# Optimization experiments

Hardware: AMD Instinct MI355X
Metric: run time of the kernel (lower is better)

Reference implementation:

```python
import jax, jax.numpy as jnp
import numpy as np

L = 5      # n_levels
NH = 4     # num_heads
P = 4      # num_points
E = 256    # embed_dims
C = 256    # bev_dims
HB = 128
WB = 128
NQ = HB * WB
HD = E // NH
NL = 6     # num_layers
FF = 2 * E # ffn hidden


def setup_inputs() -> dict:
    key = jax.random.key(0)
    ks = jax.random.split(key, 12)
    s = 0.02
    def n(k, shape):
        return jax.random.normal(k, shape, jnp.float32) * s
    return dict(
        feat_bev=jax.random.normal(ks[0], (L, 1, C, HB, WB), jnp.float32),
        norm0_g=jnp.ones((L, C), jnp.float32), norm0_b=jnp.zeros((L, C), jnp.float32),
        in_w=n(ks[1], (C * L, E)), in_b=jnp.zeros((E,), jnp.float32),
        pos_row=n(ks[2], (HB, E // 2)), pos_col=n(ks[3], (WB, E // 2)),
        off_w=n(ks[4], (NL, E, NH * L * P * 2)), off_b=n(ks[5], (NL, NH * L * P * 2)),
        aw_w=n(ks[6], (NL, E, NH * L * P)), aw_b=jnp.zeros((NL, NH * L * P), jnp.float32),
        val_w=n(ks[7], (NL, C, E)), val_b=jnp.zeros((NL, E), jnp.float32),
        out_w=n(ks[8], (NL, E, E)), out_b=jnp.zeros((NL, E), jnp.float32),
        ln1_g=jnp.ones((NL, E), jnp.float32), ln1_b=jnp.zeros((NL, E), jnp.float32),
        ln2_g=jnp.ones((NL, E), jnp.float32), ln2_b=jnp.zeros((NL, E), jnp.float32),
        ffn_w1=n(ks[9], (NL, E, FF)), ffn_b1=jnp.zeros((NL, FF), jnp.float32),
        ffn_w2=n(ks[10], (NL, FF, E)), ffn_b2=jnp.zeros((NL, E), jnp.float32),
    )


def _ln(x, g, b):
    m = x.mean(-1, keepdims=True)
    v = ((x - m) ** 2).mean(-1, keepdims=True)
    return (x - m) * jax.lax.rsqrt(v + 1e-5) * g + b


def reference(feat_bev, norm0_g, norm0_b, in_w, in_b, pos_row, pos_col,
              off_w, off_b, aw_w, aw_b, val_w, val_b, out_w, out_b,
              ln1_g, ln1_b, ln2_g, ln2_b, ffn_w1, ffn_b1, ffn_w2, ffn_b2):
    Lv, bs, Cc, H, W = feat_bev.shape
    nq = H * W
    # per-level LN over channels (norm_layer0)
    f = feat_bev.transpose(0, 1, 3, 4, 2).reshape(Lv, bs, nq, Cc)
    f = _ln(f, norm0_g[:, None, None, :], norm0_b[:, None, None, :])  # [L, bs, nq, C]
    # input_proj on channel-concat of levels (level-major block rows of in_w)
    q = jnp.einsum('lbnc,lce->bne', f, in_w.reshape(Lv, Cc, E)) + in_b  # [bs, nq, E]
    # learned positional encoding: pos[h, w] = cat(col[w], row[h])
    pos = jnp.concatenate([
        jnp.broadcast_to(pos_col[None, :, :], (H, W, E // 2)),
        jnp.broadcast_to(pos_row[:, None, :], (H, W, E // 2))], -1).reshape(1, nq, E)
    # reference points (pixel centers, normalized)
    ys, xs = jnp.meshgrid(jnp.arange(H, dtype=jnp.float32) + 0.5,
                          jnp.arange(W, dtype=jnp.float32) + 0.5, indexing='ij')
    ref = jnp.stack([xs.ravel() / W, ys.ravel() / H], -1)  # [nq, 2] (x, y)
    norm = jnp.array([W, H], jnp.float32)
    b_ix = jnp.arange(bs)[:, None, None, None, None]
    h_ix = jnp.arange(NH)[None, None, :, None, None]
    l_ix = jnp.arange(Lv)[None, None, None, :, None]
    for i in range(NL):
        qp = q + pos
        off = (qp @ off_w[i] + off_b[i]).reshape(bs, nq, NH, Lv, P, 2)
        aw = jax.nn.softmax((qp @ aw_w[i] + aw_b[i]).reshape(bs, nq, NH, Lv * P), -1)
        aw = aw.reshape(bs, nq, NH, Lv, P)
        loc = ref[None, :, None, None, None, :] + off / norm
        x = loc[..., 0] * W - 0.5
        y = loc[..., 1] * H - 0.5
        x0 = jnp.floor(x); y0 = jnp.floor(y)
        fx = x - x0; fy = y - y0
        x0i = x0.astype(jnp.int32); y0i = y0.astype(jnp.int32)
        # per-layer value projection of normed multi-level features
        val = (jnp.einsum('lbnc,ce->blne', f, val_w[i]) + val_b[i]).reshape(bs, Lv, nq, NH, HD)
        acc = jnp.zeros((bs, nq, NH, HD), q.dtype)
        for dx, dy, wgt in ((0, 0, (1 - fx) * (1 - fy)), (1, 0, fx * (1 - fy)),
                            (0, 1, (1 - fx) * fy), (1, 1, fx * fy)):
            ix = x0i + dx; iy = y0i + dy
            valid = ((ix >= 0) & (ix < W) & (iy >= 0) & (iy < H)).astype(q.dtype)
            sidx = jnp.clip(iy, 0, H - 1) * W + jnp.clip(ix, 0, W - 1)
            g = val[b_ix, l_ix, sidx, h_ix]  # [bs, nq, NH, Lv, P, HD]
            acc = acc + jnp.einsum('bqhlp,bqhlpd->bqhd', wgt * valid * aw, g)
        q = q + (acc.reshape(bs, nq, NH * HD) @ out_w[i] + out_b[i])
        q = _ln(q, ln1_g[i], ln1_b[i])
        q = q + jax.nn.relu(q @ ffn_w1[i] + ffn_b1[i]) @ ffn_w2[i] + ffn_b2[i]
        q = _ln(q, ln2_g[i], ln2_b[i])
    return q.transpose(0, 2, 1).reshape(bs, E, H, W)
```

## Files before the change

kernel.cpp:

```cpp
#include <hip/hip_runtime.h>
#include <hip/hip_bf16.h>
#include <stdint.h>

static constexpr int kL  = 5;
static constexpr int kNH = 4;
static constexpr int kP  = 4;
static constexpr int kE  = 256;
static constexpr int kC  = 256;
static constexpr int kH  = 128;
static constexpr int kW  = 128;
static constexpr int kNQ = kH * kW;
static constexpr int kNL = 6;
static constexpr int kFF = 2 * kE;
static constexpr int kCOMB = 240;

typedef short bf16x8 __attribute__((ext_vector_type(8)));
typedef float f32x4 __attribute__((ext_vector_type(4)));

__device__ __forceinline__ short f2bf(float x) {
  union { float f; uint32_t u; } v; v.f = x;
  uint32_t r = v.u + 0x7fffu + ((v.u >> 16) & 1u);
  return (short)(r >> 16);
}
__device__ __forceinline__ uint32_t pack2(float a, float b) {
  return (uint32_t)(unsigned short)f2bf(a) | ((uint32_t)(unsigned short)f2bf(b) << 16);
}
__device__ __forceinline__ float bflo(uint32_t u) { return __uint_as_float(u << 16); }
__device__ __forceinline__ float bfhi(uint32_t u) { return __uint_as_float(u & 0xffff0000u); }
__device__ __forceinline__ float bf2f(unsigned short u) {
  return __uint_as_float((uint32_t)u << 16);
}

__device__ __forceinline__ void gl_lds16(const void* g, void* l) {
  __builtin_amdgcn_global_load_lds(
      (const __attribute__((address_space(1))) void*)g,
      (__attribute__((address_space(3))) void*)l, 16, 0, 0);
}

template <int BM, int MODE, int RB>
__global__ __launch_bounds__(512, MODE == 0 ? 4 : 2) void gemm2_kernel(
    const short* __restrict__ A, long sAb, int lda,
    const short* __restrict__ BT, int ldbt, int Kb, int nbatch,
    const float* __restrict__ bias,
    float* Cf, short* __restrict__ Cb, int ldc, int relu, long zouts,
    const float* __restrict__ pos_row, const float* __restrict__ pos_col,
    const short* __restrict__ w2BT, const float* __restrict__ w2B,
    short* __restrict__ out2) {
  static_assert(BM == 64, "layout assumes BM=64");
  constexpr bool FUSED = (MODE == 5);
  constexpr int BK = 64;
  constexpr int KG = 2;
  constexpr int NW = 8;
  constexpr int MT = 2;
  constexpr int NT = 4;
  constexpr int AG = (BM / 16) * KG;
  constexpr int BG = 16 * KG;
  constexpr int ASZ = BM * BK;
  constexpr int BSZ = 256 * BK;
  __shared__ short smem[2 * ASZ + 2 * BSZ + (FUSED ? 64 * 280 : 0)];
  short* const Asm = smem;
  short* const Bsm = smem + 2 * ASZ;
  short* const qpS = smem + 2 * ASZ + 2 * BSZ;
  const int tid = threadIdx.x;
  const int wave = tid >> 6, lane = tid & 63;
  const int wy = wave >> 2, wx = wave & 3;
  const long row0 = (long)blockIdx.y * BM;
  const int col0 = blockIdx.x * 256;
  const int srow = lane >> 2;
  const int skof = ((lane & 3) ^ (srow & 3)) * 8;
  const int fr = lane & 15, fq = lane >> 4;
  const int ua = (fr * 4 + (fq ^ (fr & 3))) * 8;
  f32x4 acc[MT][NT] = {};
  const int KT = Kb >> 6;
  const int NTILES = nbatch * KT;

  auto stage_tile = [&](int buf, int bb, int kt) {
    const short* Ab = A + (long)bb * sAb + row0 * lda;
    const short* Bb = BT + (long)col0 * ldbt + (long)bb * Kb;
    int k0 = kt * BK;
#pragma unroll
    for (int t = wave; t < AG + BG; t += NW) {
      if (t < AG) {
        int rg = t >> 1, kg = t & 1;
        gl_lds16(Ab + (long)(rg * 16 + srow) * lda + k0 + kg * 32 + skof,
                 &Asm[buf * ASZ + t * 512]);
      } else {
        int u = t - AG;
        int rg = u >> 1, kg = u & 1;
        gl_lds16(Bb + (long)(rg * 16 + srow) * ldbt + k0 + kg * 32 + skof,
                 &Bsm[buf * BSZ + u * 512]);
      }
    }
  };

  int cur = 0;
  stage_tile(0, 0, 0);
  __syncthreads();
  int sb = 0, sk = 0;
  for (int idx = 0; idx < NTILES; ++idx) {
    if (idx + 1 < NTILES) {
      if (++sk == KT) { sk = 0; ++sb; }
      stage_tile(cur ^ 1, sb, sk);
    }
#pragma unroll
    for (int kk = 0; kk < KG; ++kk) {
      bf16x8 af[MT], bfv[NT];
#pragma unroll
      for (int t = 0; t < MT; ++t)
        af[t] = *(const bf16x8*)&Asm[cur * ASZ + ((wy * MT + t) * KG + kk) * 512 + ua];
#pragma unroll
      for (int t = 0; t < NT; ++t)
        bfv[t] = *(const bf16x8*)&Bsm[cur * BSZ + ((wx * 4 + t) * KG + kk) * 512 + ua];
#pragma unroll
      for (int mt = 0; mt < MT; ++mt)
#pragma unroll
        for (int nt = 0; nt < NT; ++nt)
          acc[mt][nt] = __builtin_amdgcn_mfma_f32_16x16x32_bf16(
              af[mt], bfv[nt], acc[mt][nt], 0, 0, 0);
    }
    __syncthreads();
    cur ^= 1;
  }

  const int colb = col0 + wx * 64 + fr;
  const long rowb = row0 + wy * 32 + fq * 4;

  if (MODE == 0) {
    const long zoff = (long)blockIdx.x * zouts;
#pragma unroll
    for (int mt = 0; mt < MT; ++mt)
#pragma unroll
      for (int rr = 0; rr < 4; ++rr) {
        long row = rowb + mt * 16 + rr;
#pragma unroll
        for (int nt = 0; nt < NT; ++nt) {
          int col = colb + nt * 16;
          float v = acc[mt][nt][rr] + bias[col];
          if (relu) v = fmaxf(v, 0.f);
          if (Cf) Cf[row * ldc + col] = v;
          if (Cb) Cb[zoff + row * ldc + col] = f2bf(v);
        }
      }
  } else if (MODE == 5) {
#pragma unroll
    for (int mt = 0; mt < MT; ++mt)
#pragma unroll
      for (int rr = 0; rr < 4; ++rr) {
        long row = rowb + mt * 16 + rr;
        int rl = wy * 32 + mt * 16 + fq * 4 + rr;
        int wpos = (int)row & (kW - 1), hpos = (int)row >> 7;
#pragma unroll
        for (int nt = 0; nt < NT; ++nt) {
          int col = colb + nt * 16;
          float v = acc[mt][nt][rr] + bias[col];
          Cf[row * 256 + col] = v;
          float pv = (col < 128) ? pos_col[wpos * 128 + col]
                                 : pos_row[hpos * 128 + (col - 128)];
          qpS[rl * 280 + col] = f2bf(v + pv);
        }
      }
  }
  if constexpr (FUSED) {
    auto stageW = [&](int buf, int t2) {
      int k0 = (t2 & 3) * BK;
#pragma unroll
      for (int u = wave; u < BG; u += NW) {
        int rg = u >> 1, kg = u & 1;
        gl_lds16(w2BT + (long)(rg * 16 + srow) * 256 + k0 + kg * 32 + skof,
                 &Bsm[buf * BSZ + u * 512]);
      }
    };
    f32x4 acc2[4][NT] = {};
    stageW(cur, 0);
    __syncthreads();
    for (int t2 = 0; t2 < 4; ++t2) {
      if (t2 + 1 < 4) stageW(cur ^ 1, t2 + 1);
      int k0 = t2 * BK;
#pragma unroll
      for (int kk = 0; kk < KG; ++kk) {
        bf16x8 av[4], bv[NT];
#pragma unroll
        for (int mt = 0; mt < 4; ++mt)
          av[mt] = *(const bf16x8*)&qpS[(mt * 16 + fr) * 280 + k0 +
                                        kk * 32 + fq * 8];
#pragma unroll
        for (int t = 0; t < NT; ++t)
          bv[t] = *(const bf16x8*)&Bsm[cur * BSZ + ((wx * 4 + t) * KG + kk) *
                                           512 + ua];
#pragma unroll
        for (int mt = 0; mt < 4; ++mt)
#pragma unroll
          for (int t = 0; t < NT; ++t)
            acc2[mt][t] = __builtin_amdgcn_mfma_f32_16x16x32_bf16(
                av[mt], bv[t], acc2[mt][t], 0, 0, 0);
      }
      __syncthreads();
      cur ^= 1;
    }
#pragma unroll
    for (int mt = 0; mt < 4; ++mt)
#pragma unroll
      for (int rr = 0; rr < 4; ++rr) {
        long row = row0 + mt * 16 + fq * 4 + rr;
#pragma unroll
        for (int nt = 0; nt < NT; ++nt) {
          int oc = wx * 64 + nt * 16 + fr;
          out2[row * 256 + oc] = f2bf(acc2[mt][nt][rr] + w2B[oc]);
        }
      }
  }
}

template <int LAST>
__global__ __launch_bounds__(512, 2) void layer_kernel(
    const short* __restrict__ accb, const short* __restrict__ outTW,
    const float* __restrict__ outb, float* __restrict__ q,
    const float* __restrict__ ln1g, const float* __restrict__ ln1b,
    const short* __restrict__ f1T, const float* __restrict__ f1b,
    short* __restrict__ hid, const short* __restrict__ f2T,
    const float* __restrict__ f2b, const float* __restrict__ ln2g,
    const float* __restrict__ ln2b, const float* __restrict__ pos_row,
    const float* __restrict__ pos_col, const short* __restrict__ combTW,
    const float* __restrict__ comb_b, short* __restrict__ comb_bf) {
  constexpr int BK = 64, KG = 2, NW = 8, MT = 2, NT = 4;
  constexpr int AG = 8, BG = 32;
  constexpr int ASZ = 64 * BK, BSZ = 256 * BK;
  __shared__ short smem[2 * ASZ + 2 * BSZ + 64 * 280];
  short* const Asm = smem;
  short* const Bsm = smem + 2 * ASZ;
  short* const qpS = smem + 2 * ASZ + 2 * BSZ;
  float2* const lnpart = (float2*)Asm;
  const int tid = threadIdx.x;
  const int wave = tid >> 6, lane = tid & 63;
  const int wy = wave >> 2, wx = wave & 3;
  const long row0 = (long)blockIdx.y * 64;
  const int srow = lane >> 2;
  const int skof = ((lane & 3) ^ (srow & 3)) * 8;
  const int fr = lane & 15, fq = lane >> 4;
  const int ua = (fr * 4 + (fq ^ (fr & 3))) * 8;
  const int colb = wx * 64 + fr;
  const long rowb = row0 + wy * 32 + fq * 4;
  f32x4 acc[MT][NT];

  auto run_gemm = [&](const short* Ab, int lda, const short* Bb, int ldbt,
                      int ntiles) {
#pragma unroll
    for (int mt = 0; mt < MT; ++mt)
#pragma unroll
      for (int nt = 0; nt < NT; ++nt) acc[mt][nt] = f32x4{0.f, 0.f, 0.f, 0.f};
    auto stage = [&](int buf, int kt) {
      int k0 = kt * BK;
#pragma unroll
      for (int t = wave; t < AG + BG; t += NW) {
        if (t < AG) {
          int rg = t >> 1, kg = t & 1;
          gl_lds16(Ab + (long)(rg * 16 + srow) * lda + k0 + kg * 32 + skof,
                   &Asm[buf * ASZ + t * 512]);
        } else {
          int u = t - AG, rg = u >> 1, kg = u & 1;
          gl_lds16(Bb + (long)(rg * 16 + srow) * ldbt + k0 + kg * 32 + skof,
                   &Bsm[buf * BSZ + u * 512]);
        }
      }
    };
    stage(0, 0);
    __syncthreads();
    int cur = 0;
    for (int t = 0; t < ntiles; ++t) {
      if (t + 1 < ntiles) stage(cur ^ 1, t + 1);
#pragma unroll
      for (int kk = 0; kk < KG; ++kk) {
        bf16x8 af[MT], bfv[NT];
#pragma unroll
        for (int i = 0; i < MT; ++i)
          af[i] = *(const bf16x8*)&Asm[cur * ASZ +
                                       ((wy * MT + i) * KG + kk) * 512 + ua];
#pragma unroll
        for (int i = 0; i < NT; ++i)
          bfv[i] = *(const bf16x8*)&Bsm[cur * BSZ +
                                        ((wx * 4 + i) * KG + kk) * 512 + ua];
#pragma unroll
        for (int mt = 0; mt < MT; ++mt)
#pragma unroll
          for (int nt = 0; nt < NT; ++nt)
            acc[mt][nt] = __builtin_amdgcn_mfma_f32_16x16x32_bf16(
                af[mt], bfv[nt], acc[mt][nt], 0, 0, 0);
      }
      __syncthreads();
      cur ^= 1;
    }
  };

  auto ln_epilogue = [&](const float* bias, auto residf, const float* g,
                         const float* b, auto writer) {
#pragma unroll
    for (int mt = 0; mt < MT; ++mt)
#pragma unroll
      for (int rr = 0; rr < 4; ++rr) {
        long row = rowb + mt * 16 + rr;
        int rl = wy * 32 + mt * 16 + fq * 4 + rr;
        float s = 0.f, s2 = 0.f;
#pragma unroll
        for (int nt = 0; nt < NT; ++nt) {
          int col = colb + nt * 16;
          float v = acc[mt][nt][rr] + bias[col] + residf(row, col, rl);
          acc[mt][nt][rr] = v;
          s += v; s2 += v * v;
        }
#pragma unroll
        for (int o = 8; o > 0; o >>= 1) {
          s += __shfl_xor(s, o);
          s2 += __shfl_xor(s2, o);
        }
        if (fr == 0) lnpart[rl * 4 + wx] = make_float2(s, s2);
      }
    __syncthreads();
#pragma unroll
    for (int mt = 0; mt < MT; ++mt)
#pragma unroll
      for (int rr = 0; rr < 4; ++rr) {
        int rl = wy * 32 + mt * 16 + fq * 4 + rr;
        long row = rowb + mt * 16 + rr;
        float s = 0.f, s2 = 0.f;
#pragma unroll
        for (int c = 0; c < 4; ++c) {
          s += lnpart[rl * 4 + c].x;
          s2 += lnpart[rl * 4 + c].y;
        }
        float m = s * (1.f / 256);
        float var = s2 * (1.f / 256) - m * m;
        float rs = rsqrtf(var + 1e-5f);
#pragma unroll
        for (int nt = 0; nt < NT; ++nt) {
          int col = colb + nt * 16;
          float y = (acc[mt][nt][rr] - m) * rs * g[col] + b[col];
          writer(rl, row, col, y);
        }
      }
  };

  auto run_gemm2 = [&](const short* WT, int nhalf, int ld2, bool dorelu,
                       const float* b2, short* out2) {
    auto stageW = [&](int buf, int t2) {
      int hf = t2 >> 2, k0 = (t2 & 3) * BK;
#pragma unroll
      for (int u = wave; u < BG; u += NW) {
        int rg = u >> 1, kg = u & 1;
        gl_lds16(WT + (long)(hf * 256 + rg * 16 + srow) * 256 + k0 + kg * 32 +
                     skof,
                 &Bsm[buf * BSZ + u * 512]);
      }
    };
    const int NT2 = nhalf * 4;
    f32x4 acc2[4][NT];
#pragma unroll
    for (int mt = 0; mt < 4; ++mt)
#pragma unroll
      for (int t = 0; t < NT; ++t) acc2[mt][t] = f32x4{0.f, 0.f, 0.f, 0.f};
    stageW(0, 0);
    __syncthreads();
    int cur = 0;
    for (int t2 = 0; t2 < NT2; ++t2) {
      if (t2 + 1 < NT2) stageW(cur ^ 1, t2 + 1);
      int k0 = (t2 & 3) * BK;
#pragma unroll
      for (int kk = 0; kk < KG; ++kk) {
        bf16x8 av[4], bv[NT];
#pragma unroll
        for (int mt = 0; mt < 4; ++mt)
          av[mt] = *(const bf16x8*)&qpS[(mt * 16 + fr) * 280 + k0 + kk * 32 +
                                        fq * 8];
#pragma unroll
        for (int t = 0; t < NT; ++t)
          bv[t] = *(const bf16x8*)&Bsm[cur * BSZ +
                                       ((wx * 4 + t) * KG + kk) * 512 + ua];
#pragma unroll
        for (int mt = 0; mt < 4; ++mt)
#pragma unroll
          for (int t = 0; t < NT; ++t)
            acc2[mt][t] = __builtin_amdgcn_mfma_f32_16x16x32_bf16(
                av[mt], bv[t], acc2[mt][t], 0, 0, 0);
      }
      if ((t2 & 3) == 3) {
        int hf = t2 >> 2;
#pragma unroll
        for (int mt = 0; mt < 4; ++mt)
#pragma unroll
          for (int rr = 0; rr < 4; ++rr) {
            long row = row0 + mt * 16 + fq * 4 + rr;
#pragma unroll
            for (int nt = 0; nt < NT; ++nt) {
              int oc = hf * 256 + wx * 64 + nt * 16 + fr;
              float v = acc2[mt][nt][rr] + b2[oc];
              if (dorelu) v = fmaxf(v, 0.f);
              out2[row * ld2 + oc] = f2bf(v);
            }
          }
#pragma unroll
        for (int mt = 0; mt < 4; ++mt)
#pragma unroll
          for (int t = 0; t < NT; ++t) acc2[mt][t] = f32x4{0.f, 0.f, 0.f, 0.f};
      }
      __syncthreads();
      cur ^= 1;
    }
  };

  run_gemm(accb + row0 * 256, 256, outTW, 256, 4);
  ln_epilogue(
      outb, [&](long row, int col, int) { return q[row * 256 + col]; }, ln1g,
      ln1b,
      [&](int rl, long row, int col, float y) { qpS[rl * 280 + col] = f2bf(y); });
  run_gemm2(f1T, 2, 512, true, f1b, hid);
  run_gemm(hid + row0 * 512, 512, f2T, 512, 8);
  ln_epilogue(
      f2b,
      [&](long row, int col, int rl) {
        return bf2f((unsigned short)qpS[rl * 280 + col]);
      },
      ln2g, ln2b,
      [&](int rl, long row, int col, float y) {
        q[row * 256 + col] = y;
        if (!LAST) {
          int wpos = (int)row & (kW - 1), hpos = (int)row >> 7;
          float pv = (col < 128) ? pos_col[wpos * 128 + col]
                                 : pos_row[hpos * 128 + (col - 128)];
          qpS[rl * 280 + col] = f2bf(y + pv);
        }
      });
  if (!LAST) run_gemm2(combTW, 1, 256, false, comb_b, comb_bf);
}

__global__ __launch_bounds__(256) void convert_all_kernel(
    const float* __restrict__ in_w, const float* __restrict__ val_w,
    const float* __restrict__ out_w, const float* __restrict__ ffn_w1,
    const float* __restrict__ ffn_w2, const float* __restrict__ off_w,
    const float* __restrict__ aw_w, const float* __restrict__ off_b,
    const float* __restrict__ aw_b,
    short* __restrict__ inT, short* __restrict__ valT, short* __restrict__ outT,
    short* __restrict__ ffn1T, short* __restrict__ ffn2T,
    short* __restrict__ combT, float* __restrict__ comb_bias) {
  long e = (long)blockIdx.x * 256 + threadIdx.x;
  if (e < 327680) {
    int idx = (int)e;
    int n = idx / 1280, k = idx - n * 1280;
    inT[idx] = f2bf(in_w[(long)k * 256 + n]);
    return;
  }
  e -= 327680;
  if (e < 393216) {
    int z = (int)(e >> 16), idx = (int)e & 65535;
    int n = idx >> 8, k = idx & 255;
    valT[e] = f2bf(val_w[((long)z * 256 + k) * 256 + n]);
    return;
  }
  e -= 393216;
  if (e < 393216) {
    int z = (int)(e >> 16), idx = (int)e & 65535;
    int n = idx >> 8, k = idx & 255;
    outT[e] = f2bf(out_w[((long)z * 256 + k) * 256 + n]);
    return;
  }
  e -= 393216;
  if (e < 786432) {
    int z = (int)(e / 131072);
    int idx = (int)(e - (long)z * 131072);
    int n = idx >> 8, k = idx & 255;
    ffn1T[e] = f2bf(ffn_w1[((long)z * 256 + k) * 512 + n]);
    return;
  }
  e -= 786432;
  if (e < 786432) {
    int z = (int)(e / 131072);
    int idx = (int)(e - (long)z * 131072);
    int n = idx >> 9, k = idx & 511;
    ffn2T[e] = f2bf(ffn_w2[((long)z * 512 + k) * 256 + n]);
    return;
  }
  e -= 786432;
  {
    int z = (int)(e >> 16), idx = (int)e & 65535;
    int n = idx >> 8, k = idx & 255;
    float v = 0.f;
    if (n < 160) v = off_w[((long)z * 256 + k) * 160 + n];
    else if (n < kCOMB) v = aw_w[((long)z * 256 + k) * 80 + (n - 160)];
    combT[e] = f2bf(v);
    if (k == 0)
      comb_bias[z * 256 + n] =
          (n < 160) ? off_b[z * 160 + n]
                    : (n < kCOMB ? aw_b[z * 80 + (n - 160)] : 0.f);
  }
}

__global__ __launch_bounds__(256) void ln_fused_kernel(
    const float* __restrict__ feat, const float* __restrict__ g,
    const float* __restrict__ b, short* __restrict__ f) {
  __shared__ float tile[256][33];
  __shared__ float2 part[8][32];
  __shared__ float mS[32], rsS[32];
  int l = blockIdx.y;
  int n0 = blockIdx.x * 32;
  int tx = threadIdx.x & 31;
  int ty = threadIdx.x >> 5;
  float s = 0.f, s2 = 0.f;
#pragma unroll 8
  for (int j = 0; j < 32; ++j) {
    int c = ty * 32 + j;
    float v = feat[((long)(l * kC + c)) * kNQ + n0 + tx];
    tile[c][tx] = v;
    s += v; s2 += v * v;
  }
  part[ty][tx] = make_float2(s, s2);
  __syncthreads();
  if (ty == 0) {
    float ss = 0.f, ss2 = 0.f;
#pragma unroll
    for (int j = 0; j < 8; ++j) {
      ss += part[j][tx].x; ss2 += part[j][tx].y;
    }
    float m = ss * (1.f / kC);
    float var = ss2 * (1.f / kC) - m * m;
    mS[tx] = m;
    rsS[tx] = rsqrtf(var + 1e-5f);
  }
  __syncthreads();
  int c = threadIdx.x;
  float gv = g[l * kC + c], bv = b[l * kC + c];
#pragma unroll 8
  for (int r = 0; r < 32; ++r) {
    float v = (tile[c][r] - mS[r]) * rsS[r] * gv + bv;
    f[((long)l * kNQ + n0 + r) * kC + c] = f2bf(v);
  }
}

__global__ __launch_bounds__(256) void sample_kernel(
    const unsigned short* __restrict__ comb, const short* __restrict__ val,
    short* __restrict__ accb) {
  __shared__ float2 ic[4][2][4][85];
  int wv = threadIdx.x >> 6;
  int lane = threadIdx.x & 63;
  int half = lane >> 5;
  int hl = lane & 31;
  int n = blockIdx.x * 8 + wv * 2 + half;
  int wq = n & (kW - 1);
  int hq = n >> 7;
  const unsigned short* cb = comb + (long)n * 256;
#pragma unroll
  for (int h = 0; h < 4; ++h) {
    float raw = (hl < 20) ? bf2f(cb[160 + h * 20 + hl]) : -1e30f;
    float mx = raw;
#pragma unroll
    for (int o = 16; o > 0; o >>= 1) mx = fmaxf(mx, __shfl_xor(mx, o));
    float ev = (hl < 20) ? __expf(raw - mx) : 0.f;
    float se = ev;
#pragma unroll
    for (int o = 16; o > 0; o >>= 1) se += __shfl_xor(se, o);
    if (hl < 20) {
      float awv = ev / se;
      int l = hl >> 2;
      float ox = bf2f(cb[h * 40 + hl * 2 + 0]);
      float oy = bf2f(cb[h * 40 + hl * 2 + 1]);
      float x = (float)wq + ox;
      float y = (float)hq + oy;
      float x0f = floorf(x), y0f = floorf(y);
      float fx = x - x0f, fy = y - y0f;
      int x0 = (int)x0f, y0 = (int)y0f;
#pragma unroll
      for (int c = 0; c < 4; ++c) {
        int dx = c & 1, dy = c >> 1;
        int ix = x0 + dx, iy = y0 + dy;
        float wgt = (dx ? fx : 1.f - fx) * (dy ? fy : 1.f - fy);
        bool valid = (ix >= 0 && ix < kW && iy >= 0 && iy < kH);
        int cix = min(max(ix, 0), kW - 1);
        int ciy = min(max(iy, 0), kH - 1);
        int sidx = ciy * kW + cix;
        int byteoff = (l * kNQ + sidx) * (kE * 2);
        float coef = valid ? awv * wgt : 0.f;
        ic[wv][half][h][hl * 4 + c] = make_float2(__int_as_float(byteoff), coef);
      }
    }
  }
  __syncthreads();
  int h2 = (lane >> 3) & 3;
  int ch8 = (lane & 7) * 8;
  const char* vb = (const char*)val + (h2 * 64 + ch8) * 2;
  const float2* icp = &ic[wv][half][h2][0];
  float a0 = 0.f, a1 = 0.f, a2 = 0.f, a3 = 0.f;
  float a4 = 0.f, a5 = 0.f, a6 = 0.f, a7 = 0.f;
#pragma unroll 4
  for (int j = 0; j < 80; ++j) {
    float2 oc = icp[j];
    int off = __float_as_int(oc.x);
    uint4 u = *(const uint4*)(vb + off);
    float cf = oc.y;
    a0 += cf * bflo(u.x); a1 += cf * bfhi(u.x);
    a2 += cf * bflo(u.y); a3 += cf * bfhi(u.y);
    a4 += cf * bflo(u.z); a5 += cf * bfhi(u.z);
    a6 += cf * bflo(u.w); a7 += cf * bfhi(u.w);
  }
  uint4 o;
  o.x = pack2(a0, a1); o.y = pack2(a2, a3);
  o.z = pack2(a4, a5); o.w = pack2(a6, a7);
  *(uint4*)(accb + (long)n * kE + h2 * 64 + ch8) = o;
}

__global__ __launch_bounds__(256) void transpose_kernel(
    const float* __restrict__ q, float* __restrict__ out) {
  __shared__ float t[32][33];
  int eb = blockIdx.x * 32, nb = blockIdx.y * 32;
  int tx = threadIdx.x & 31, ty = threadIdx.x >> 5;
#pragma unroll
  for (int j = 0; j < 4; ++j)
    t[ty + j * 8][tx] = q[(long)(nb + ty + j * 8) * kE + eb + tx];
  __syncthreads();
#pragma unroll
  for (int j = 0; j < 4; ++j)
    out[(long)(eb + ty + j * 8) * kNQ + nb + tx] = t[tx][ty + j * 8];
}

extern "C" void kernel_launch(void* const* d_in, const int* in_sizes, int n_in,
                              void* d_out, int out_size, void* d_ws,
                              size_t ws_size, hipStream_t stream) {
  const float* feat    = (const float*)d_in[0];
  const float* norm0_g = (const float*)d_in[1];
  const float* norm0_b = (const float*)d_in[2];
  const float* in_w    = (const float*)d_in[3];
  const float* in_b    = (const float*)d_in[4];
  const float* pos_row = (const float*)d_in[5];
  const float* pos_col = (const float*)d_in[6];
  const float* off_w   = (const float*)d_in[7];
  const float* off_b   = (const float*)d_in[8];
  const float* aw_w    = (const float*)d_in[9];
  const float* aw_b    = (const float*)d_in[10];
  const float* val_w   = (const float*)d_in[11];
  const float* val_b   = (const float*)d_in[12];
  const float* out_w   = (const float*)d_in[13];
  const float* out_b   = (const float*)d_in[14];
  const float* ln1_g   = (const float*)d_in[15];
  const float* ln1_b   = (const float*)d_in[16];
  const float* ln2_g   = (const float*)d_in[17];
  const float* ln2_b   = (const float*)d_in[18];
  const float* ffn_w1  = (const float*)d_in[19];
  const float* ffn_b1  = (const float*)d_in[20];
  const float* ffn_w2  = (const float*)d_in[21];
  const float* ffn_b2  = (const float*)d_in[22];

  char* p = (char*)d_ws;
  auto alloc = [&](size_t bytes) -> char* {
    char* r = p;
    p += (bytes + 255) & ~(size_t)255;
    return r;
  };
  const size_t valSlab = (size_t)kL * kNQ * kE;
  short* f_bf    = (short*)alloc((size_t)kL * kNQ * kC * 2);
  short* val_bf  = (short*)alloc(3 * valSlab * 2);
  float* q       = (float*)alloc((size_t)kNQ * kE * 4);
  short* accb    = (short*)alloc((size_t)kNQ * kE * 2);
  short* hid_bf  = (short*)alloc((size_t)kNQ * kFF * 2);
  short* comb_bf = (short*)alloc((size_t)kNQ * 256 * 2);
  float* comb_b  = (float*)alloc((size_t)kNL * 256 * 4);
  short* inT     = (short*)alloc((size_t)256 * 1280 * 2);
  short* valT    = (short*)alloc((size_t)kNL * 256 * 256 * 2);
  short* outT    = (short*)alloc((size_t)kNL * 256 * 256 * 2);
  short* ffn1T   = (short*)alloc((size_t)kNL * 512 * 256 * 2);
  short* ffn2T   = (short*)alloc((size_t)kNL * 256 * 512 * 2);
  short* combT   = (short*)alloc((size_t)kNL * 256 * 256 * 2);

  convert_all_kernel<<<12032, 256, 0, stream>>>(
      in_w, val_w, out_w, ffn_w1, ffn_w2, off_w, aw_w, off_b, aw_b,
      inT, valT, outT, ffn1T, ffn2T, combT, comb_b);

  ln_fused_kernel<<<dim3(kNQ / 32, kL), 256, 0, stream>>>(feat, norm0_g,
                                                          norm0_b, f_bf);

  const long zouts = (long)kL * kNQ * 256 - 256;
  gemm2_kernel<64, 0, 0><<<dim3(3, kL * kNQ / 64), 512, 0, stream>>>(
      f_bf, 0, kC, valT, 256, 256, 1, val_b,
      nullptr, val_bf, kE, 0, zouts, nullptr, nullptr,
      nullptr, nullptr, nullptr);

  gemm2_kernel<64, 5, 0><<<dim3(1, kNQ / 64), 512, 0, stream>>>(
      f_bf, (long)kNQ * kC, kC, inT, 1280, 256, kL, in_b,
      q, nullptr, 256, 0, 0, pos_row, pos_col, combT, comb_b, comb_bf);

  for (int i = 0; i < kNL; ++i) {
    const short* outT_i  = outT + (long)i * 256 * 256;
    const short* f1T_i   = ffn1T + (long)i * 512 * 256;
    const short* f2T_i   = ffn2T + (long)i * 256 * 512;

    sample_kernel<<<kNQ / 8, 256, 0, stream>>>(
        (const unsigned short*)comb_bf, val_bf + (long)(i % 3) * valSlab,
        accb);
    if (i == 2) {
      gemm2_kernel<64, 0, 0><<<dim3(3, kL * kNQ / 64), 512, 0, stream>>>(
          f_bf, 0, kC, valT + 3 * 256 * 256, 256, 256, 1, val_b + 3 * kE,
          nullptr, val_bf, kE, 0, zouts, nullptr, nullptr,
          nullptr, nullptr, nullptr);
    }
    if (i + 1 < kNL) {
      layer_kernel<0><<<dim3(1, kNQ / 64), 512, 0, stream>>>(
          accb, outT_i, out_b + (long)i * kE, q,
          ln1_g + (long)i * kE, ln1_b + (long)i * kE,
          f1T_i, ffn_b1 + (long)i * kFF, hid_bf,
          f2T_i, ffn_b2 + (long)i * kE,
          ln2_g + (long)i * kE, ln2_b + (long)i * kE,
          pos_row, pos_col,
          combT + (long)(i + 1) * 256 * 256, comb_b + (i + 1) * 256, comb_bf);
    } else {
      layer_kernel<1><<<dim3(1, kNQ / 64), 512, 0, stream>>>(
          accb, outT_i, out_b + (long)i * kE, q,
          ln1_g + (long)i * kE, ln1_b + (long)i * kE,
          f1T_i, ffn_b1 + (long)i * kFF, hid_bf,
          f2T_i, ffn_b2 + (long)i * kE,
          ln2_g + (long)i * kE, ln2_b + (long)i * kE,
          pos_row, pos_col, nullptr, nullptr, nullptr);
    }
  }

  transpose_kernel<<<dim3(kE / 32, kNQ / 32), 256, 0, stream>>>(q,
                                                                (float*)d_out);
}
```

Before: 868.3 us.

## Fuse deformable sampling into layer kernel and feed output-projection GEMM from LDS

```diff
diff --git a/kernel.cpp b/kernel.cpp
--- a/kernel.cpp
+++ b/kernel.cpp
@@ -213,8 +213,9 @@
 
 template <int LAST>
 __global__ __launch_bounds__(512, 2) void layer_kernel(
-    const short* __restrict__ accb, const short* __restrict__ outTW,
-    const float* __restrict__ outb, float* __restrict__ q,
+    const unsigned short* __restrict__ comb, const short* __restrict__ val,
+    const short* __restrict__ outTW, const float* __restrict__ outb,
+    float* __restrict__ q,
     const float* __restrict__ ln1g, const float* __restrict__ ln1b,
     const short* __restrict__ f1T, const float* __restrict__ f1b,
     short* __restrict__ hid, const short* __restrict__ f2T,
@@ -229,6 +230,8 @@
   short* const Asm = smem;
   short* const Bsm = smem + 2 * ASZ;
   short* const qpS = smem + 2 * ASZ + 2 * BSZ;
+  short* const accS = qpS;
+  float2* const ic = (float2*)Bsm;
   float2* const lnpart = (float2*)Asm;
   const int tid = threadIdx.x;
   const int wave = tid >> 6, lane = tid & 63;
@@ -242,6 +245,127 @@
   const long rowb = row0 + wy * 32 + fq * 4;
   f32x4 acc[MT][NT];
 
+  {
+    const int half = lane >> 5;
+    const int hl = lane & 31;
+    const int h2 = (lane >> 3) & 3;
+    const int ch8 = (lane & 7) * 8;
+    const int ch = h2 * 64 + ch8;
+    const char* vb = (const char*)val + ch * 2;
+    for (int pass = 0; pass < 4; ++pass) {
+      int nl = wave * 8 + pass * 2 + half;
+      long n = row0 + nl;
+      int wq = (int)n & (kW - 1), hq = (int)n >> 7;
+      const unsigned short* cb = comb + n * 256;
+      float2* icw = ic + (long)(wave * 2 + half) * 4 * 85;
+#pragma unroll
+      for (int h = 0; h < 4; ++h) {
+        float raw = (hl < 20) ? bf2f(cb[160 + h * 20 + hl]) : -1e30f;
+        float mx = raw;
+#pragma unroll
+        for (int o = 16; o > 0; o >>= 1) mx = fmaxf(mx, __shfl_xor(mx, o));
+        float ev = (hl < 20) ? __expf(raw - mx) : 0.f;
+        float se = ev;
+#pragma unroll
+        for (int o = 16; o > 0; o >>= 1) se += __shfl_xor(se, o);
+        if (hl < 20) {
+          float awv = ev / se;
+          int l = hl >> 2;
+          float ox = bf2f(cb[h * 40 + hl * 2 + 0]);
+          float oy = bf2f(cb[h * 40 + hl * 2 + 1]);
+          float x = (float)wq + ox;
+          float y = (float)hq + oy;
+          float x0f = floorf(x), y0f = floorf(y);
+          float fx = x - x0f, fy = y - y0f;
+          int x0 = (int)x0f, y0 = (int)y0f;
+#pragma unroll
+          for (int c = 0; c < 4; ++c) {
+            int dx = c & 1, dy = c >> 1;
+            int ix = x0 + dx, iy = y0 + dy;
+            float wgt = (dx ? fx : 1.f - fx) * (dy ? fy : 1.f - fy);
+            bool valid = (ix >= 0 && ix < kW && iy >= 0 && iy < kH);
+            int cix = min(max(ix, 0), kW - 1);
+            int ciy = min(max(iy, 0), kH - 1);
+            int sidx = ciy * kW + cix;
+            int byteoff = (l * kNQ + sidx) * (kE * 2);
+            float coef = valid ? awv * wgt : 0.f;
+            icw[h * 85 + hl * 4 + c] =
+                make_float2(__int_as_float(byteoff), coef);
+          }
+        }
+      }
+      __syncthreads();
+      const float2* icp = ic + ((long)(wave * 2 + half) * 4 + h2) * 85;
+      float a0 = 0.f, a1 = 0.f, a2 = 0.f, a3 = 0.f;
+      float a4 = 0.f, a5 = 0.f, a6 = 0.f, a7 = 0.f;
+#pragma unroll 4
+      for (int j = 0; j < 80; ++j) {
+        float2 oc = icp[j];
+        int off = __float_as_int(oc.x);
+        uint4 u = *(const uint4*)(vb + off);
+        float cf = oc.y;
+        a0 += cf * bflo(u.x); a1 += cf * bfhi(u.x);
+        a2 += cf * bflo(u.y); a3 += cf * bfhi(u.y);
+        a4 += cf * bflo(u.z); a5 += cf * bfhi(u.z);
+        a6 += cf * bflo(u.w); a7 += cf * bfhi(u.w);
+      }
+      uint4 o;
+      o.x = pack2(a0, a1); o.y = pack2(a2, a3);
+      o.z = pack2(a4, a5); o.w = pack2(a6, a7);
+      int rg = nl >> 4, sr = nl & 15, kg = ch >> 5, quad = (ch >> 3) & 3;
+      *(uint4*)&accS[(rg * 8 + kg) * 512 + (sr * 4 + (quad ^ (sr & 3))) * 8] = o;
+    }
+  }
+  __syncthreads();
+
+  auto ln_epilogue = [&](const float* bias, auto residf, const float* g,
+                         const float* b, auto writer) {
+#pragma unroll
+    for (int mt = 0; mt < MT; ++mt)
+#pragma unroll
+      for (int rr = 0; rr < 4; ++rr) {
+        long row = rowb + mt * 16 + rr;
+        int rl = wy * 32 + mt * 16 + fq * 4 + rr;
+        float s = 0.f, s2 = 0.f;
+#pragma unroll
+        for (int nt = 0; nt < NT; ++nt) {
+          int col = colb + nt * 16;
+          float v = acc[mt][nt][rr] + bias[col] + residf(row, col, rl);
+          acc[mt][nt][rr] = v;
+          s += v; s2 += v * v;
+        }
+#pragma unroll
+        for (int o = 8; o > 0; o >>= 1) {
+          s += __shfl_xor(s, o);
+          s2 += __shfl_xor(s2, o);
+        }
+        if (fr == 0) lnpart[rl * 4 + wx] = make_float2(s, s2);
+      }
+    __syncthreads();
+#pragma unroll
+    for (int mt = 0; mt < MT; ++mt)
+#pragma unroll
+      for (int rr = 0; rr < 4; ++rr) {
+        int rl = wy * 32 + mt * 16 + fq * 4 + rr;
+        long row = rowb + mt * 16 + rr;
+        float s = 0.f, s2 = 0.f;
+#pragma unroll
+        for (int c = 0; c < 4; ++c) {
+          s += lnpart[rl * 4 + c].x;
+          s2 += lnpart[rl * 4 + c].y;
+        }
+        float m = s * (1.f / 256);
+        float var = s2 * (1.f / 256) - m * m;
+        float rs = rsqrtf(var + 1e-5f);
+#pragma unroll
+        for (int nt = 0; nt < NT; ++nt) {
+          int col = colb + nt * 16;
+          float y = (acc[mt][nt][rr] - m) * rs * g[col] + b[col];
+          writer(rl, row, col, y);
+        }
+      }
+  };
+
   auto run_gemm = [&](const short* Ab, int lda, const short* Bb, int ldbt,
                       int ntiles) {
 #pragma unroll
@@ -291,54 +415,6 @@
     }
   };
 
-  auto ln_epilogue = [&](const float* bias, auto residf, const float* g,
-                         const float* b, auto writer) {
-#pragma unroll
-    for (int mt = 0; mt < MT; ++mt)
-#pragma unroll
-      for (int rr = 0; rr < 4; ++rr) {
-        long row = rowb + mt * 16 + rr;
-        int rl = wy * 32 + mt * 16 + fq * 4 + rr;
-        float s = 0.f, s2 = 0.f;
-#pragma unroll
-        for (int nt = 0; nt < NT; ++nt) {
-          int col = colb + nt * 16;
-          float v = acc[mt][nt][rr] + bias[col] + residf(row, col, rl);
-          acc[mt][nt][rr] = v;
-          s += v; s2 += v * v;
-        }
-#pragma unroll
-        for (int o = 8; o > 0; o >>= 1) {
-          s += __shfl_xor(s, o);
-          s2 += __shfl_xor(s2, o);
-        }
-        if (fr == 0) lnpart[rl * 4 + wx] = make_float2(s, s2);
-      }
-    __syncthreads();
-#pragma unroll
-    for (int mt = 0; mt < MT; ++mt)
-#pragma unroll
-      for (int rr = 0; rr < 4; ++rr) {
-        int rl = wy * 32 + mt * 16 + fq * 4 + rr;
-        long row = rowb + mt * 16 + rr;
-        float s = 0.f, s2 = 0.f;
-#pragma unroll
-        for (int c = 0; c < 4; ++c) {
-          s += lnpart[rl * 4 + c].x;
-          s2 += lnpart[rl * 4 + c].y;
-        }
-        float m = s * (1.f / 256);
-        float var = s2 * (1.f / 256) - m * m;
-        float rs = rsqrtf(var + 1e-5f);
-#pragma unroll
-        for (int nt = 0; nt < NT; ++nt) {
-          int col = colb + nt * 16;
-          float y = (acc[mt][nt][rr] - m) * rs * g[col] + b[col];
-          writer(rl, row, col, y);
-        }
-      }
-  };
-
   auto run_gemm2 = [&](const short* WT, int nhalf, int ld2, bool dorelu,
                        const float* b2, short* out2) {
     auto stageW = [&](int buf, int t2) {
@@ -406,7 +482,47 @@
     }
   };
 
-  run_gemm(accb + row0 * 256, 256, outTW, 256, 4);
+  {
+#pragma unroll
+    for (int mt = 0; mt < MT; ++mt)
+#pragma unroll
+      for (int nt = 0; nt < NT; ++nt) acc[mt][nt] = f32x4{0.f, 0.f, 0.f, 0.f};
+    auto stageB = [&](int buf, int kt) {
+      int k0 = kt * BK;
+#pragma unroll
+      for (int u = wave; u < BG; u += NW) {
+        int rg = u >> 1, kg = u & 1;
+        gl_lds16(outTW + (long)(rg * 16 + srow) * 256 + k0 + kg * 32 + skof,
+                 &Bsm[buf * BSZ + u * 512]);
+      }
+    };
+    stageB(0, 0);
+    __syncthreads();
+    int cur = 0;
+    for (int kt = 0; kt < 4; ++kt) {
+      if (kt < 3) stageB(cur ^ 1, kt + 1);
+#pragma unroll
+      for (int kk = 0; kk < KG; ++kk) {
+        bf16x8 af[MT], bfv[NT];
+#pragma unroll
+        for (int i = 0; i < MT; ++i)
+          af[i] = *(const bf16x8*)&accS[((wy * 2 + i) * 8 + kt * 2 + kk) * 512 +
+                                        ua];
+#pragma unroll
+        for (int i = 0; i < NT; ++i)
+          bfv[i] = *(const bf16x8*)&Bsm[cur * BSZ +
+                                        ((wx * 4 + i) * KG + kk) * 512 + ua];
+#pragma unroll
+        for (int mt = 0; mt < MT; ++mt)
+#pragma unroll
+          for (int nt = 0; nt < NT; ++nt)
+            acc[mt][nt] = __builtin_amdgcn_mfma_f32_16x16x32_bf16(
+                af[mt], bfv[nt], acc[mt][nt], 0, 0, 0);
+      }
+      __syncthreads();
+      cur ^= 1;
+    }
+  }
   ln_epilogue(
       outb, [&](long row, int col, int) { return q[row * 256 + col]; }, ln1g,
       ln1b,
@@ -531,77 +647,6 @@
     float v = (tile[c][r] - mS[r]) * rsS[r] * gv + bv;
     f[((long)l * kNQ + n0 + r) * kC + c] = f2bf(v);
   }
-}
-
-__global__ __launch_bounds__(256) void sample_kernel(
-    const unsigned short* __restrict__ comb, const short* __restrict__ val,
-    short* __restrict__ accb) {
-  __shared__ float2 ic[4][2][4][85];
-  int wv = threadIdx.x >> 6;
-  int lane = threadIdx.x & 63;
-  int half = lane >> 5;
-  int hl = lane & 31;
-  int n = blockIdx.x * 8 + wv * 2 + half;
-  int wq = n & (kW - 1);
-  int hq = n >> 7;
-  const unsigned short* cb = comb + (long)n * 256;
-#pragma unroll
-  for (int h = 0; h < 4; ++h) {
-    float raw = (hl < 20) ? bf2f(cb[160 + h * 20 + hl]) : -1e30f;
-    float mx = raw;
-#pragma unroll
-    for (int o = 16; o > 0; o >>= 1) mx = fmaxf(mx, __shfl_xor(mx, o));
-    float ev = (hl < 20) ? __expf(raw - mx) : 0.f;
-    float se = ev;
-#pragma unroll
-    for (int o = 16; o > 0; o >>= 1) se += __shfl_xor(se, o);
-    if (hl < 20) {
-      float awv = ev / se;
-      int l = hl >> 2;
-      float ox = bf2f(cb[h * 40 + hl * 2 + 0]);
-      float oy = bf2f(cb[h * 40 + hl * 2 + 1]);
-      float x = (float)wq + ox;
-      float y = (float)hq + oy;
-      float x0f = floorf(x), y0f = floorf(y);
-      float fx = x - x0f, fy = y - y0f;
-      int x0 = (int)x0f, y0 = (int)y0f;
-#pragma unroll
-      for (int c = 0; c < 4; ++c) {
-        int dx = c & 1, dy = c >> 1;
-        int ix = x0 + dx, iy = y0 + dy;
-        float wgt = (dx ? fx : 1.f - fx) * (dy ? fy : 1.f - fy);
-        bool valid = (ix >= 0 && ix < kW && iy >= 0 && iy < kH);
-        int cix = min(max(ix, 0), kW - 1);
-        int ciy = min(max(iy, 0), kH - 1);
-        int sidx = ciy * kW + cix;
-        int byteoff = (l * kNQ + sidx) * (kE * 2);
-        float coef = valid ? awv * wgt : 0.f;
-        ic[wv][half][h][hl * 4 + c] = make_float2(__int_as_float(byteoff), coef);
-      }
-    }
-  }
-  __syncthreads();
-  int h2 = (lane >> 3) & 3;
-  int ch8 = (lane & 7) * 8;
-  const char* vb = (const char*)val + (h2 * 64 + ch8) * 2;
-  const float2* icp = &ic[wv][half][h2][0];
-  float a0 = 0.f, a1 = 0.f, a2 = 0.f, a3 = 0.f;
-  float a4 = 0.f, a5 = 0.f, a6 = 0.f, a7 = 0.f;
-#pragma unroll 4
-  for (int j = 0; j < 80; ++j) {
-    float2 oc = icp[j];
-    int off = __float_as_int(oc.x);
-    uint4 u = *(const uint4*)(vb + off);
-    float cf = oc.y;
-    a0 += cf * bflo(u.x); a1 += cf * bfhi(u.x);
-    a2 += cf * bflo(u.y); a3 += cf * bfhi(u.y);
-    a4 += cf * bflo(u.z); a5 += cf * bfhi(u.z);
-    a6 += cf * bflo(u.w); a7 += cf * bfhi(u.w);
-  }
-  uint4 o;
-  o.x = pack2(a0, a1); o.y = pack2(a2, a3);
-  o.z = pack2(a4, a5); o.w = pack2(a6, a7);
-  *(uint4*)(accb + (long)n * kE + h2 * 64 + ch8) = o;
 }
 
 __global__ __launch_bounds__(256) void transpose_kernel(
@@ -655,7 +700,6 @@
   short* f_bf    = (short*)alloc((size_t)kL * kNQ * kC * 2);
   short* val_bf  = (short*)alloc(3 * valSlab * 2);
   float* q       = (float*)alloc((size_t)kNQ * kE * 4);
-  short* accb    = (short*)alloc((size_t)kNQ * kE * 2);
   short* hid_bf  = (short*)alloc((size_t)kNQ * kFF * 2);
   short* comb_bf = (short*)alloc((size_t)kNQ * 256 * 2);
   float* comb_b  = (float*)alloc((size_t)kNL * 256 * 4);
@@ -688,10 +732,7 @@
     const short* f1T_i   = ffn1T + (long)i * 512 * 256;
     const short* f2T_i   = ffn2T + (long)i * 256 * 512;
 
-    sample_kernel<<<kNQ / 8, 256, 0, stream>>>(
-        (const unsigned short*)comb_bf, val_bf + (long)(i % 3) * valSlab,
-        accb);
-    if (i == 2) {
+    if (i == 3) {
       gemm2_kernel<64, 0, 0><<<dim3(3, kL * kNQ / 64), 512, 0, stream>>>(
           f_bf, 0, kC, valT + 3 * 256 * 256, 256, 256, 1, val_b + 3 * kE,
           nullptr, val_bf, kE, 0, zouts, nullptr, nullptr,
@@ -699,7 +740,8 @@
     }
     if (i + 1 < kNL) {
       layer_kernel<0><<<dim3(1, kNQ / 64), 512, 0, stream>>>(
-          accb, outT_i, out_b + (long)i * kE, q,
+          (const unsigned short*)comb_bf, val_bf + (long)(i % 3) * valSlab,
+          outT_i, out_b + (long)i * kE, q,
           ln1_g + (long)i * kE, ln1_b + (long)i * kE,
           f1T_i, ffn_b1 + (long)i * kFF, hid_bf,
           f2T_i, ffn_b2 + (long)i * kE,
@@ -708,7 +750,8 @@
           combT + (long)(i + 1) * 256 * 256, comb_b + (i + 1) * 256, comb_bf);
     } else {
       layer_kernel<1><<<dim3(1, kNQ / 64), 512, 0, stream>>>(
-          accb, outT_i, out_b + (long)i * kE, q,
+          (const unsigned short*)comb_bf, val_bf + (long)(i % 3) * valSlab,
+          outT_i, out_b + (long)i * kE, q,
           ln1_g + (long)i * kE, ln1_b + (long)i * kE,
           f1T_i, ffn_b1 + (long)i * kFF, hid_bf,
           f2T_i, ffn_b2 + (long)i * kE,
```

After: 984.0 us. 1.13x slower.

## Keep FFN hidden activations in LDS and split second-stage GEMMs across wave rows

Applied to the files above, without the earlier changes.

```diff
diff --git a/kernel.cpp b/kernel.cpp
--- a/kernel.cpp
+++ b/kernel.cpp
@@ -162,7 +162,7 @@
   }
   if constexpr (FUSED) {
     auto stageW = [&](int buf, int t2) {
-      int k0 = (t2 & 3) * BK;
+      int k0 = t2 * BK;
 #pragma unroll
       for (int u = wave; u < BG; u += NW) {
         int rg = u >> 1, kg = u & 1;
@@ -170,7 +170,7 @@
                  &Bsm[buf * BSZ + u * 512]);
       }
     };
-    f32x4 acc2[4][NT] = {};
+    f32x4 acc2[MT][NT] = {};
     stageW(cur, 0);
     __syncthreads();
     for (int t2 = 0; t2 < 4; ++t2) {
@@ -178,17 +178,17 @@
       int k0 = t2 * BK;
 #pragma unroll
       for (int kk = 0; kk < KG; ++kk) {
-        bf16x8 av[4], bv[NT];
-#pragma unroll
-        for (int mt = 0; mt < 4; ++mt)
-          av[mt] = *(const bf16x8*)&qpS[(mt * 16 + fr) * 280 + k0 +
+        bf16x8 av[MT], bv[NT];
+#pragma unroll
+        for (int mt = 0; mt < MT; ++mt)
+          av[mt] = *(const bf16x8*)&qpS[(wy * 32 + mt * 16 + fr) * 280 + k0 +
                                         kk * 32 + fq * 8];
 #pragma unroll
         for (int t = 0; t < NT; ++t)
           bv[t] = *(const bf16x8*)&Bsm[cur * BSZ + ((wx * 4 + t) * KG + kk) *
                                            512 + ua];
 #pragma unroll
-        for (int mt = 0; mt < 4; ++mt)
+        for (int mt = 0; mt < MT; ++mt)
 #pragma unroll
           for (int t = 0; t < NT; ++t)
             acc2[mt][t] = __builtin_amdgcn_mfma_f32_16x16x32_bf16(
@@ -198,10 +198,10 @@
       cur ^= 1;
     }
 #pragma unroll
-    for (int mt = 0; mt < 4; ++mt)
+    for (int mt = 0; mt < MT; ++mt)
 #pragma unroll
       for (int rr = 0; rr < 4; ++rr) {
-        long row = row0 + mt * 16 + fq * 4 + rr;
+        long row = row0 + wy * 32 + mt * 16 + fq * 4 + rr;
 #pragma unroll
         for (int nt = 0; nt < NT; ++nt) {
           int oc = wx * 64 + nt * 16 + fr;
@@ -217,19 +217,20 @@
     const float* __restrict__ outb, float* __restrict__ q,
     const float* __restrict__ ln1g, const float* __restrict__ ln1b,
     const short* __restrict__ f1T, const float* __restrict__ f1b,
-    short* __restrict__ hid, const short* __restrict__ f2T,
-    const float* __restrict__ f2b, const float* __restrict__ ln2g,
-    const float* __restrict__ ln2b, const float* __restrict__ pos_row,
-    const float* __restrict__ pos_col, const short* __restrict__ combTW,
-    const float* __restrict__ comb_b, short* __restrict__ comb_bf) {
+    const short* __restrict__ f2T, const float* __restrict__ f2b,
+    const float* __restrict__ ln2g, const float* __restrict__ ln2b,
+    const float* __restrict__ pos_row, const float* __restrict__ pos_col,
+    const short* __restrict__ combTW, const float* __restrict__ comb_b,
+    short* __restrict__ comb_bf) {
   constexpr int BK = 64, KG = 2, NW = 8, MT = 2, NT = 4;
   constexpr int AG = 8, BG = 32;
   constexpr int ASZ = 64 * BK, BSZ = 256 * BK;
-  __shared__ short smem[2 * ASZ + 2 * BSZ + 64 * 280];
+  __shared__ short smem[64 * 280 + 2 * BSZ + 64 * 280];
   short* const Asm = smem;
-  short* const Bsm = smem + 2 * ASZ;
-  short* const qpS = smem + 2 * ASZ + 2 * BSZ;
-  float2* const lnpart = (float2*)Asm;
+  short* const hS  = smem;
+  short* const Bsm = smem + 64 * 280;
+  short* const qpS = smem + 64 * 280 + 2 * BSZ;
+  float2* const lnpart = (float2*)smem;
   const int tid = threadIdx.x;
   const int wave = tid >> 6, lane = tid & 63;
   const int wy = wave >> 2, wx = wave & 3;
@@ -291,6 +292,46 @@
     }
   };
 
+  auto ldsA_gemm = [&](const short* As_lds, const short* WT, int ldw,
+                       int kofs, f32x4(&dst)[MT][NT]) {
+    auto stg = [&](int buf, int t2) {
+      int k0 = kofs + t2 * BK;
+#pragma unroll
+      for (int u = wave; u < BG; u += NW) {
+        int rg = u >> 1, kg = u & 1;
+        gl_lds16(WT + (long)(rg * 16 + srow) * ldw + k0 + kg * 32 + skof,
+                 &Bsm[buf * BSZ + u * 512]);
+      }
+    };
+    stg(0, 0);
+    __syncthreads();
+    int cur = 0;
+    for (int t2 = 0; t2 < 4; ++t2) {
+      if (t2 + 1 < 4) stg(cur ^ 1, t2 + 1);
+      int k0 = t2 * BK;
+#pragma unroll
+      for (int kk = 0; kk < KG; ++kk) {
+        bf16x8 av[MT], bv[NT];
+#pragma unroll
+        for (int mt = 0; mt < MT; ++mt)
+          av[mt] = *(const bf16x8*)&As_lds[(wy * 32 + mt * 16 + fr) * 280 +
+                                           k0 + kk * 32 + fq * 8];
+#pragma unroll
+        for (int t = 0; t < NT; ++t)
+          bv[t] = *(const bf16x8*)&Bsm[cur * BSZ +
+                                       ((wx * 4 + t) * KG + kk) * 512 + ua];
+#pragma unroll
+        for (int mt = 0; mt < MT; ++mt)
+#pragma unroll
+          for (int t = 0; t < NT; ++t)
+            dst[mt][t] = __builtin_amdgcn_mfma_f32_16x16x32_bf16(
+                av[mt], bv[t], dst[mt][t], 0, 0, 0);
+      }
+      __syncthreads();
+      cur ^= 1;
+    }
+  };
+
   auto ln_epilogue = [&](const float* bias, auto residf, const float* g,
                          const float* b, auto writer) {
 #pragma unroll
@@ -339,80 +380,35 @@
       }
   };
 
-  auto run_gemm2 = [&](const short* WT, int nhalf, int ld2, bool dorelu,
-                       const float* b2, short* out2) {
-    auto stageW = [&](int buf, int t2) {
-      int hf = t2 >> 2, k0 = (t2 & 3) * BK;
-#pragma unroll
-      for (int u = wave; u < BG; u += NW) {
-        int rg = u >> 1, kg = u & 1;
-        gl_lds16(WT + (long)(hf * 256 + rg * 16 + srow) * 256 + k0 + kg * 32 +
-                     skof,
-                 &Bsm[buf * BSZ + u * 512]);
-      }
-    };
-    const int NT2 = nhalf * 4;
-    f32x4 acc2[4][NT];
-#pragma unroll
-    for (int mt = 0; mt < 4; ++mt)
-#pragma unroll
-      for (int t = 0; t < NT; ++t) acc2[mt][t] = f32x4{0.f, 0.f, 0.f, 0.f};
-    stageW(0, 0);
-    __syncthreads();
-    int cur = 0;
-    for (int t2 = 0; t2 < NT2; ++t2) {
-      if (t2 + 1 < NT2) stageW(cur ^ 1, t2 + 1);
-      int k0 = (t2 & 3) * BK;
-#pragma unroll
-      for (int kk = 0; kk < KG; ++kk) {
-        bf16x8 av[4], bv[NT];
-#pragma unroll
-        for (int mt = 0; mt < 4; ++mt)
-          av[mt] = *(const bf16x8*)&qpS[(mt * 16 + fr) * 280 + k0 + kk * 32 +
-                                        fq * 8];
-#pragma unroll
-        for (int t = 0; t < NT; ++t)
-          bv[t] = *(const bf16x8*)&Bsm[cur * BSZ +
-                                       ((wx * 4 + t) * KG + kk) * 512 + ua];
-#pragma unroll
-        for (int mt = 0; mt < 4; ++mt)
-#pragma unroll
-          for (int t = 0; t < NT; ++t)
-            acc2[mt][t] = __builtin_amdgcn_mfma_f32_16x16x32_bf16(
-                av[mt], bv[t], acc2[mt][t], 0, 0, 0);
-      }
-      if ((t2 & 3) == 3) {
-        int hf = t2 >> 2;
-#pragma unroll
-        for (int mt = 0; mt < 4; ++mt)
-#pragma unroll
-          for (int rr = 0; rr < 4; ++rr) {
-            long row = row0 + mt * 16 + fq * 4 + rr;
-#pragma unroll
-            for (int nt = 0; nt < NT; ++nt) {
-              int oc = hf * 256 + wx * 64 + nt * 16 + fr;
-              float v = acc2[mt][nt][rr] + b2[oc];
-              if (dorelu) v = fmaxf(v, 0.f);
-              out2[row * ld2 + oc] = f2bf(v);
-            }
-          }
-#pragma unroll
-        for (int mt = 0; mt < 4; ++mt)
-#pragma unroll
-          for (int t = 0; t < NT; ++t) acc2[mt][t] = f32x4{0.f, 0.f, 0.f, 0.f};
-      }
-      __syncthreads();
-      cur ^= 1;
-    }
-  };
-
   run_gemm(accb + row0 * 256, 256, outTW, 256, 4);
   ln_epilogue(
       outb, [&](long row, int col, int) { return q[row * 256 + col]; }, ln1g,
       ln1b,
       [&](int rl, long row, int col, float y) { qpS[rl * 280 + col] = f2bf(y); });
-  run_gemm2(f1T, 2, 512, true, f1b, hid);
-  run_gemm(hid + row0 * 512, 512, f2T, 512, 8);
+  __syncthreads();
+
+#pragma unroll
+  for (int mt = 0; mt < MT; ++mt)
+#pragma unroll
+    for (int nt = 0; nt < NT; ++nt) acc[mt][nt] = f32x4{0.f, 0.f, 0.f, 0.f};
+  for (int hf = 0; hf < 2; ++hf) {
+    f32x4 a1[MT][NT] = {};
+    ldsA_gemm(qpS, f1T + (long)(hf * 256) * 256, 256, 0, a1);
+#pragma unroll
+    for (int mt = 0; mt < MT; ++mt)
+#pragma unroll
+      for (int rr = 0; rr < 4; ++rr) {
+        int rl = wy * 32 + mt * 16 + fq * 4 + rr;
+#pragma unroll
+        for (int nt = 0; nt < NT; ++nt) {
+          int col = colb + nt * 16;
+          float v = a1[mt][nt][rr] + f1b[hf * 256 + col];
+          hS[rl * 280 + col] = f2bf(fmaxf(v, 0.f));
+        }
+      }
+    __syncthreads();
+    ldsA_gemm(hS, f2T, 512, hf * 256, acc);
+  }
   ln_epilogue(
       f2b,
       [&](long row, int col, int rl) {
@@ -428,7 +424,22 @@
           qpS[rl * 280 + col] = f2bf(y + pv);
         }
       });
-  if (!LAST) run_gemm2(combTW, 1, 256, false, comb_b, comb_bf);
+  if (!LAST) {
+    __syncthreads();
+    f32x4 a2[MT][NT] = {};
+    ldsA_gemm(qpS, combTW, 256, 0, a2);
+#pragma unroll
+    for (int mt = 0; mt < MT; ++mt)
+#pragma unroll
+      for (int rr = 0; rr < 4; ++rr) {
+        long row = row0 + wy * 32 + mt * 16 + fq * 4 + rr;
+#pragma unroll
+        for (int nt = 0; nt < NT; ++nt) {
+          int oc = wx * 64 + nt * 16 + fr;
+          comb_bf[row * 256 + oc] = f2bf(a2[mt][nt][rr] + comb_b[oc]);
+        }
+      }
+  }
 }
 
 __global__ __launch_bounds__(256) void convert_all_kernel(
@@ -656,7 +667,6 @@
   short* val_bf  = (short*)alloc(3 * valSlab * 2);
   float* q       = (float*)alloc((size_t)kNQ * kE * 4);
   short* accb    = (short*)alloc((size_t)kNQ * kE * 2);
-  short* hid_bf  = (short*)alloc((size_t)kNQ * kFF * 2);
   short* comb_bf = (short*)alloc((size_t)kNQ * 256 * 2);
   float* comb_b  = (float*)alloc((size_t)kNL * 256 * 4);
   short* inT     = (short*)alloc((size_t)256 * 1280 * 2);
@@ -701,7 +711,7 @@
       layer_kernel<0><<<dim3(1, kNQ / 64), 512, 0, stream>>>(
           accb, outT_i, out_b + (long)i * kE, q,
           ln1_g + (long)i * kE, ln1_b + (long)i * kE,
-          f1T_i, ffn_b1 + (long)i * kFF, hid_bf,
+          f1T_i, ffn_b1 + (long)i * kFF,
           f2T_i, ffn_b2 + (long)i * kE,
           ln2_g + (long)i * kE, ln2_b + (long)i * kE,
           pos_row, pos_col,
@@ -710,7 +720,7 @@
       layer_kernel<1><<<dim3(1, kNQ / 64), 512, 0, stream>>>(
           accb, outT_i, out_b + (long)i * kE, q,
           ln1_g + (long)i * kE, ln1_b + (long)i * kE,
-          f1T_i, ffn_b1 + (long)i * kFF, hid_bf,
+          f1T_i, ffn_b1 + (long)i * kFF,
           f2T_i, ffn_b2 + (long)i * kE,
           ln2_g + (long)i * kE, ln2_b + (long)i * kE,
           pos_row, pos_col, nullptr, nullptr, nullptr);
```

After: 822.6 us. 1.06x faster.
